# Optimization experiments

Measured on AMD Instinct MI355X. Metric: run time of the kernel, lower is better.

Reference implementation:

```python
import jax, jax.numpy as jnp
import numpy as np

B, FDIM, T, N, TOPK = 64, 80, 400, 5, 2
EPS = 1e-5


def conv2d(x, w, stride, pad):
    return jax.lax.conv_general_dilated(
        x, w, window_strides=stride,
        padding=[(pad, pad), (pad, pad)],
        dimension_numbers=('NCHW', 'OIHW', 'NCHW'))


def bn2d(x, g, b):
    # eval-mode BatchNorm2d with running_mean=0, running_var=1
    s = g / jnp.sqrt(1.0 + EPS)
    return x * s[None, :, None, None] + b[None, :, None, None]


def gelu(x):
    return jax.nn.gelu(x, approximate=False)  # torch nn.GELU default (erf)


def setup_inputs() -> dict:
    key = jax.random.key(0)
    ks = jax.random.split(key, 12)

    def rn(k, shape, scale=0.05):
        return jax.random.normal(k, shape, dtype=jnp.float32) * scale

    return {
        'x': rn(ks[0], (B, 1, FDIM, T, N), 1.0),
        'total': rn(ks[1], (B, 1, FDIM, 5 * T), 1.0),
        'gw1': rn(ks[2], (32, 1, 5, 15)),
        'g1': jnp.ones((32,), jnp.float32), 'b1': jnp.zeros((32,), jnp.float32),
        'gw2': rn(ks[3], (64, 32, 5, 15)),
        'g2': jnp.ones((64,), jnp.float32), 'b2': jnp.zeros((64,), jnp.float32),
        'gw3': rn(ks[4], (128, 64, 5, 15)),
        'g3': jnp.ones((128,), jnp.float32), 'b3': jnp.zeros((128,), jnp.float32),
        'gw4': rn(ks[5], (256, 128, 5, 15)),
        'g4': jnp.ones((256,), jnp.float32), 'b4': jnp.zeros((256,), jnp.float32),
        'fw1': rn(ks[6], (32, 256)), 'fb1': jnp.zeros((32,), jnp.float32),
        'g1d': jnp.ones((32,), jnp.float32), 'b1d': jnp.zeros((32,), jnp.float32),
        'fw2': rn(ks[7], (5, 32)), 'fb2': jnp.zeros((5,), jnp.float32),
        'cw1': rn(ks[8], (64, 1, 7, 14)),
    }


def reference(x, total, gw1, g1, b1, gw2, g2, b2, gw3, g3, b3, gw4, g4, b4,
              fw1, fb1, g1d, b1d, fw2, fb2, cw1):
    h = gelu(bn2d(conv2d(total, gw1, (2, 4), 2), g1, b1))
    h = gelu(bn2d(conv2d(h, gw2, (2, 4), 2), g2, b2))
    h = gelu(bn2d(conv2d(h, gw3, (2, 4), 2), g3, b3))
    h = gelu(bn2d(conv2d(h, gw4, (2, 4), 2), g4, b4))
    h = h.mean(axis=(2, 3))                      # AdaptiveAvgPool2d((1,1)) + Flatten -> [B,256]
    h = gelu(h @ fw1.T + fb1)                    # Linear(256,32) + GELU
    h = h * (g1d / jnp.sqrt(1.0 + EPS)) + b1d    # eval-mode BatchNorm1d(32)
    routing_weights = h @ fw2.T + fb2            # Linear(32,5) -> [B,5]

    # ---- top-k routing ----
    probs = jax.nn.softmax(routing_weights, axis=1)
    _, sel = jax.lax.top_k(probs, TOPK)          # [B,2]
    sel = jnp.sort(sel, axis=1)
    mask = jnp.transpose(jax.nn.one_hot(sel, N, dtype=x.dtype), (0, 2, 1))  # [B,5,2]

    # ---- one-hot einsum gather + reshape + stem conv ----
    gated = jnp.einsum('bcftn,bns->bcfts', x, mask)      # [B,1,80,T,2]
    gated = gated.reshape(-1, 1, FDIM, TOPK * gated.shape[3])  # [B,1,80,2T]
    out = conv2d(gated, cw1, (2, 2), 3)                  # [B,64,40,397]
    return out, routing_weights
```

## Files before the change

### kernel.cpp

```cpp
#include <hip/hip_runtime.h>
#include <hip/hip_bf16.h>

#define DEV __device__ __forceinline__

typedef __attribute__((ext_vector_type(8))) short short8_t;
typedef __attribute__((ext_vector_type(4))) float f32x4;

DEV float gelu_erf(float x) { return 0.5f * x * (1.0f + erff(x * 0.70710678118654752440f)); }
DEV ushort f2bf(float v) { __hip_bfloat16 h = __float2bfloat16(v); return *(ushort*)&h; }

DEV int xcd_swz(int bid, int nwg) {
    int q = nwg >> 3;
    return (bid & 7) * q + (bid >> 3);
}

__global__ __launch_bounds__(256) void prep_k(
    const float* __restrict__ gw1, const float* __restrict__ gw2,
    const float* __restrict__ gw3, const float* __restrict__ gw4,
    const float* __restrict__ cw1,
    ushort* __restrict__ wp1, ushort* __restrict__ wp2,
    ushort* __restrict__ wp3, ushort* __restrict__ w4p,
    ushort* __restrict__ wp5, ushort* __restrict__ zp)
{
    __shared__ float lds[9600];
    const int tid = threadIdx.x;
    int blk = blockIdx.x;
    if (blk < 256) {
        const float* src = gw4 + (size_t)blk * 9600;
        for (int i = tid; i < 9600; i += 256) lds[i] = src[i];
        __syncthreads();
        ushort* dst = w4p + (size_t)blk * 9600;
        for (int p = tid; p < 9600; p += 256) {
            int ic = p & 127, kc = p >> 7;
            dst[p] = f2bf(lds[ic * 75 + kc]);
        }
        return;
    }
    blk -= 256;
    if (blk < 128) {
        const float* src = gw3 + (size_t)blk * 4800;
        for (int i = tid; i < 4800; i += 256) lds[i] = src[i];
        __syncthreads();
        for (int p = tid; p < 4800; p += 256) {
            int ic = p & 63, kc = p >> 6;
            wp3[(size_t)kc * 8192 + blk * 64 + ic] = f2bf(lds[ic * 75 + kc]);
        }
        return;
    }
    blk -= 128;
    if (blk < 64) {
        const float* src = gw2 + (size_t)blk * 2400;
        for (int i = tid; i < 2400; i += 256) lds[i] = src[i];
        __syncthreads();
        for (int p = tid; p < 2400; p += 256) {
            int ic = p & 31, kc = p >> 5;
            wp2[(size_t)kc * 2048 + blk * 32 + ic] = f2bf(lds[ic * 75 + kc]);
        }
        return;
    }
    for (int idx = tid; idx < 3072; idx += 256) {
        int oc = idx / 96, k = idx % 96;
        int kh = k >> 4, kw = k & 15;
        float v = (kh < 5 && kw < 15) ? gw1[oc * 75 + kh * 15 + kw] : 0.f;
        wp1[idx] = f2bf(v);
    }
    for (int idx = tid; idx < 8192; idx += 256) {
        int oc = idx >> 7, k = idx & 127;
        int kh = k >> 4, t = k & 15;
        int a = t >> 1, c = t & 1, kw = 2 * a + c - 1;
        float v = (kh < 7 && kw >= 0 && kw < 14) ? cw1[oc * 98 + kh * 14 + kw] : 0.f;
        wp5[idx] = f2bf(v);
    }
    for (int idx = tid; idx < 256; idx += 256) zp[idx] = 0;
}

template <int M_BLK, int NOC, int NCH, int NWM, int NWN, int ST, bool F32IN, bool BNG>
__global__ __launch_bounds__(64 * NWM * NWN) void convmm1_k(
    const void* __restrict__ in_, const ushort* __restrict__ wp,
    const float* __restrict__ gamma, const float* __restrict__ beta,
    void* __restrict__ out_,
    int IH, int IWE, int OH, int OW, int NOWT, int PH)
{
    constexpr int NT = 64 * NWM * NWN;
    constexpr int NR = 2 * NCH;
    constexpr int SPAN = (M_BLK - 1) * ST + 16;
    constexpr int SSTR = ((SPAN + 16 + 7) & ~7) + 8;
    constexpr int STAGE_B = NR * SSTR * 2;
    constexpr int TILE_B = BNG ? (M_BLK * NOC * 2) : (NOC * M_BLK * 4);
    constexpr int SMEM_B = STAGE_B > TILE_B ? STAGE_B : TILE_B;
    constexpr int HOFF = F32IN ? 1 : 2;
    __shared__ __align__(16) char smem[SMEM_B];
    ushort* stg = (ushort*)smem;

    int bid = xcd_swz(blockIdx.x, gridDim.x);
    const int owt = bid % NOWT; bid /= NOWT;
    const int oh = bid % OH;
    const int b  = bid / OH;
    const int ow0 = owt * M_BLK;
    const int tid = threadIdx.x;
    const int w = tid >> 6, l = tid & 63;
    const int wn = w % NWN, wm = w / NWN;
    const int m_wave = wm * 32, n_wave = wn * 32;
    const int lc = l & 15, lr = l >> 4;

    if (F32IN) {
        constexpr int NG = (SPAN + 6) / 4 + 1;
        const int iwb_al = (ow0 * ST - 2) & ~3;
        const float* inf = (const float*)in_;
        for (int u = tid; u < NR * NG; u += NT) {
            int r = u / NG, gi = u - r * NG;
            int ih = oh * 2 - PH + r;
            int iw4 = iwb_al + gi * 4;
            int q = gi * 4;
            bool rowok = (unsigned)ih < (unsigned)IH;
            if (rowok && iw4 >= 0 && iw4 + 3 < IWE) {
                float4 v = *(const float4*)&inf[((size_t)b * IH + ih) * IWE + iw4];
                ushort4 h;
                h.x = f2bf(v.x); h.y = f2bf(v.y); h.z = f2bf(v.z); h.w = f2bf(v.w);
                *(ushort4*)&stg[r * SSTR + q] = h;
            } else {
#pragma unroll
                for (int j = 0; j < 4; ++j) {
                    int iw = iw4 + j;
                    float v = (rowok && (unsigned)iw < (unsigned)IWE)
                        ? inf[((size_t)b * IH + ih) * IWE + iw] : 0.f;
                    stg[r * SSTR + q + j] = f2bf(v);
                }
            }
        }
    } else {
        constexpr int SPANU = SPAN / 2;
        constexpr int NGU = (SPANU + 6) / 4 + 1;
        const int iub_al = (ow0 - 2) & ~3;
        const uint* inu = (const uint*)in_;
        for (int u = tid; u < NR * NGU; u += NT) {
            int r = u / NGU, gi = u - r * NGU;
            int ih = oh * 2 - PH + r;
            int iu4 = iub_al + gi * 4;
            bool rowok = (unsigned)ih < (unsigned)IH;
            if (rowok && iu4 >= 0 && iu4 + 3 < IWE) {
                uint4 v = *(const uint4*)&inu[((size_t)b * IH + ih) * IWE + iu4];
                *(uint4*)&stg[r * SSTR + gi * 8] = v;
            } else {
#pragma unroll
                for (int j = 0; j < 4; ++j) {
                    int iu = iu4 + j;
                    uint v = (rowok && (unsigned)iu < (unsigned)IWE)
                        ? inu[((size_t)b * IH + ih) * IWE + iu] : 0u;
                    *(uint*)&stg[r * SSTR + gi * 8 + j * 2] = v;
                }
            }
        }
    }

    short8_t bfr[NCH][2];
    {
        const ushort* wb = wp + (size_t)(n_wave + lc) * (NCH * 32) + lr * 8;
#pragma unroll
        for (int cc = 0; cc < NCH; ++cc)
#pragma unroll
            for (int nj = 0; nj < 2; ++nj)
                bfr[cc][nj] = *(const short8_t*)(wb + (size_t)nj * 16 * (NCH * 32) + cc * 32);
    }

    __syncthreads();

    f32x4 acc[2][2];
#pragma unroll
    for (int i = 0; i < 2; ++i)
#pragma unroll
        for (int j = 0; j < 2; ++j) acc[i][j] = (f32x4){0.f, 0.f, 0.f, 0.f};

#pragma unroll
    for (int cc = 0; cc < NCH; ++cc) {
        const int kh = 2 * cc + (lr >> 1);
        const uint* lrow = (const uint*)&stg[kh * SSTR];
        short8_t a[2];
#pragma unroll
        for (int mi = 0; mi < 2; ++mi) {
            const int m = m_wave + mi * 16 + lc;
            const int half = ((m * ST + (lr & 1) * 8) >> 1) + HOFF;
            union { uint u[4]; short8_t s; } av;
            av.u[0] = lrow[half];
            av.u[1] = lrow[half + 1];
            av.u[2] = lrow[half + 2];
            av.u[3] = lrow[half + 3];
            a[mi] = av.s;
        }
#pragma unroll
        for (int mi = 0; mi < 2; ++mi)
#pragma unroll
            for (int nj = 0; nj < 2; ++nj)
                acc[mi][nj] = __builtin_amdgcn_mfma_f32_16x16x32_bf16(a[mi], bfr[cc][nj], acc[mi][nj], 0, 0, 0);
    }

    __syncthreads();

    if (BNG) {
        ushort* tile = (ushort*)smem;
#pragma unroll
        for (int nj = 0; nj < 2; ++nj) {
            const int n = n_wave + nj * 16 + lc;
            const float s = gamma[n] * rsqrtf(1.0f + 1e-5f);
            const float bb = beta[n];
#pragma unroll
            for (int mi = 0; mi < 2; ++mi)
#pragma unroll
                for (int r = 0; r < 4; ++r) {
                    const int m = m_wave + mi * 16 + lr * 4 + r;
                    float y = gelu_erf(fmaf(acc[mi][nj][r], s, bb));
                    tile[m * NOC + n] = f2bf(y);
                }
        }
        __syncthreads();
        const int mv = min(M_BLK, OW - ow0);
        uint* dst = (uint*)((ushort*)out_ + (((size_t)b * OH + oh) * OW + ow0) * NOC);
        const uint* src = (const uint*)tile;
        for (int idx = tid; idx < mv * NOC / 2; idx += NT) dst[idx] = src[idx];
    } else {
        float* tile = (float*)smem;
#pragma unroll
        for (int nj = 0; nj < 2; ++nj) {
            const int n = n_wave + nj * 16 + lc;
#pragma unroll
            for (int mi = 0; mi < 2; ++mi)
#pragma unroll
                for (int r = 0; r < 4; ++r) {
                    const int m = m_wave + mi * 16 + lr * 4 + r;
                    tile[n * M_BLK + m] = acc[mi][nj][r];
                }
        }
        __syncthreads();
        const int mv = min(M_BLK, OW - ow0);
        float* outb = (float*)out_ + ((size_t)b * NOC * OH + oh) * OW + ow0;
        for (int idx = tid; idx < NOC * mv; idx += NT) {
            int oc = idx / mv, j = idx - oc * mv;
            outb[(size_t)oc * OH * OW + j] = tile[oc * M_BLK + j];
        }
    }
}

template <int M_BLK, int OC, int ICT, int NICC, int NWM, int NWN, int UNR>
__global__ __launch_bounds__(64 * NWM * NWN) void convmm_k(
    const ushort* __restrict__ in, const ushort* __restrict__ wp,
    const float* __restrict__ gamma, const float* __restrict__ beta,
    ushort* __restrict__ out,
    int IH, int IW, int OH, int OW, int NOWT)
{
    constexpr int KH = 5, KW = 15, SW = 4;
    constexpr int MI = M_BLK / (16 * NWM);
    constexpr int NJ = OC / (16 * NWN);
    constexpr int SPAN = (M_BLK - 1) * SW + KW;
    constexpr int ICB = ICT * 2;
    constexpr int NSL = ICT / 8;
    constexpr int KEYM = NSL - 1;
    constexpr int NT = 64 * NWM * NWN;
    constexpr int NUNITS = SPAN * NSL;
    constexpr int NLD = (NUNITS + NT - 1) / NT;

    __shared__ __align__(16) ushort Abuf[SPAN * ICT];

    int bid = xcd_swz(blockIdx.x, gridDim.x);
    const int owt = bid % NOWT; bid /= NOWT;
    const int oh  = bid % OH;
    const int b   = bid / OH;
    const int ow0 = owt * M_BLK;
    const int tid = threadIdx.x;
    const int w = tid >> 6, l = tid & 63;
    const int wn = w % NWN, wm = w / NWN;
    const int m_wave = wm * (16 * MI), n_wave = wn * (16 * NJ);
    const int lc = l & 15, lr = l >> 4;

    const int ih0 = oh * 2 - 2;
    const int iw0 = ow0 * SW - 2;
    const ushort* inb = in + (size_t)b * IH * IW * ICT;

    int up[NLD], usl[NLD], uoff[NLD];
    bool uv[NLD];
#pragma unroll
    for (int i = 0; i < NLD; ++i) {
        int u = tid + i * NT;
        uv[i] = u < NUNITS;
        int uu = uv[i] ? u : 0;
        up[i] = uu / NSL;
        usl[i] = uu - up[i] * NSL;
        uoff[i] = up[i] * ICB + ((usl[i] ^ ((up[i] >> 2) & KEYM)) << 4);
    }

    uint4 rg[NLD];
    auto prefetch = [&](int kh) {
        const int ih = ih0 + kh;
        const bool rowok = (unsigned)ih < (unsigned)IH;
        const ushort* src = inb + (size_t)ih * IW * ICT;
#pragma unroll
        for (int i = 0; i < NLD; ++i) {
            int iw = iw0 + up[i];
            uint4 v = {0u, 0u, 0u, 0u};
            if (rowok && uv[i] && (unsigned)iw < (unsigned)IW)
                v = *(const uint4*)(src + (size_t)iw * ICT + usl[i] * 8);
            rg[i] = v;
        }
    };
    auto writestage = [&]() {
#pragma unroll
        for (int i = 0; i < NLD; ++i)
            if (uv[i]) *(uint4*)((char*)Abuf + uoff[i]) = rg[i];
    };

    f32x4 acc[MI][NJ];
#pragma unroll
    for (int i = 0; i < MI; ++i)
#pragma unroll
        for (int j = 0; j < NJ; ++j) acc[i][j] = (f32x4){0.f, 0.f, 0.f, 0.f};

    prefetch(0);
    writestage();
    __syncthreads();

#pragma unroll 1
    for (int kh = 0; kh < KH; ++kh) {
        if (kh + 1 < KH) prefetch(kh + 1);
        const char* buf = (const char*)Abuf;
        const ushort* wkh = wp + (size_t)(kh * KW) * OC * ICT + (size_t)(n_wave + lc) * ICT + lr * 8;
#pragma unroll UNR
        for (int kw = 0; kw < KW; ++kw) {
#pragma unroll
            for (int icc = 0; icc < NICC; ++icc) {
                short8_t a[MI], bf[NJ];
#pragma unroll
                for (int mi = 0; mi < MI; ++mi) {
                    const int r = m_wave + mi * 16 + lc;
                    const int p = SW * r + kw;
                    const int sl = icc * 4 + lr;
                    a[mi] = *(const short8_t*)(buf + p * ICB + ((sl ^ ((p >> 2) & KEYM)) << 4));
                }
                const ushort* wb = wkh + (size_t)kw * OC * ICT + icc * 32;
#pragma unroll
                for (int nj = 0; nj < NJ; ++nj)
                    bf[nj] = *(const short8_t*)(wb + (size_t)nj * 16 * ICT);
#pragma unroll
                for (int mi = 0; mi < MI; ++mi)
#pragma unroll
                    for (int nj = 0; nj < NJ; ++nj)
                        acc[mi][nj] = __builtin_amdgcn_mfma_f32_16x16x32_bf16(a[mi], bf[nj], acc[mi][nj], 0, 0, 0);
            }
        }
        if (kh + 1 < KH) {
            __syncthreads();
            writestage();
            __syncthreads();
        }
    }

    ushort* outb = out + ((size_t)b * OH + oh) * OW * OC;
#pragma unroll
    for (int nj = 0; nj < NJ; ++nj) {
        const int n = n_wave + nj * 16 + lc;
        const float s = gamma[n] * rsqrtf(1.0f + 1e-5f);
        const float bb = beta[n];
#pragma unroll
        for (int mi = 0; mi < MI; ++mi) {
#pragma unroll
            for (int r = 0; r < 4; ++r) {
                const int m = m_wave + mi * 16 + lr * 4 + r;
                const int ow = ow0 + m;
                if (ow < OW) {
                    float y = gelu_erf(fmaf(acc[mi][nj][r], s, bb));
                    outb[(size_t)ow * OC + n] = f2bf(y);
                }
            }
        }
    }
}

__global__ __launch_bounds__(256) void gemm4_k(
    const ushort* __restrict__ h3, const ushort* __restrict__ Bw,
    const ushort* __restrict__ zp, float* __restrict__ part)
{
    __shared__ __align__(16) ushort Al[3][64 * 64];
    __shared__ __align__(16) ushort Bl[3][64 * 64];
    int bid = blockIdx.x;
    const int ks = bid & 7;
    const int nt = (bid >> 3) & 3;
    const int mt = bid >> 5;
    const int m0 = mt * 64, n0 = nt * 64;
    const int k0 = (ks * 150) / 8, k1 = ((ks + 1) * 150) / 8;
    const int tid = threadIdx.x;
    const int w = tid >> 6, l = tid & 63;
    const int wr = (w >> 1) * 32, wc = (w & 1) * 32;
    const int lc = l & 15, lr = l >> 4;

    int ihb[2], iwb[2], bb[2], sspo[2];
    const ushort* gbrow[2];
#pragma unroll
    for (int i = 0; i < 2; ++i) {
        int u = tid + i * 256;
        int row = u >> 3, sl = u & 7;
        int rg = m0 + row;
        int b_ = rg / 25, p = rg - b_ * 25;
        int oh = p / 5, ow = p - oh * 5;
        bb[i] = b_;
        ihb[i] = oh * 2 - 2;
        iwb[i] = ow * 4 - 2;
        sspo[i] = (sl ^ (row & 7)) * 8;
        gbrow[i] = Bw + (size_t)(n0 + row) * 9600 + sspo[i];
    }

    auto stage = [&](int kc, int buf) {
        const int kcp = kc >> 1;
        const int kh = kcp / 15, kw = kcp - kh * 15;
        const int ice = (kc & 1) * 64;
#pragma unroll
        for (int i = 0; i < 2; ++i) {
            const int ih = ihb[i] + kh, iw = iwb[i] + kw;
            const ushort* srcA = ((unsigned)ih < 10u && (unsigned)iw < 28u)
                ? h3 + ((((size_t)bb[i] * 10 + ih) * 28 + iw) << 7) + ice + sspo[i]
                : zp;
            __builtin_amdgcn_global_load_lds(srcA, &Al[buf][(tid + i * 256) * 8], 16, 0, 0);
            __builtin_amdgcn_global_load_lds(gbrow[i] + kc * 64, &Bl[buf][(tid + i * 256) * 8], 16, 0, 0);
        }
    };

    f32x4 acc[2][2];
#pragma unroll
    for (int i = 0; i < 2; ++i)
#pragma unroll
        for (int j = 0; j < 2; ++j) acc[i][j] = (f32x4){0.f, 0.f, 0.f, 0.f};

    auto compute = [&](int buf) {
        short8_t a[2][2], bq[2][2];
#pragma unroll
        for (int mi = 0; mi < 2; ++mi)
#pragma unroll
            for (int ks_ = 0; ks_ < 2; ++ks_) {
                const int row = wr + mi * 16 + lc;
                const int sl = (ks_ * 4 + lr) ^ (row & 7);
                a[mi][ks_] = *(const short8_t*)&Al[buf][row * 64 + sl * 8];
            }
#pragma unroll
        for (int nj = 0; nj < 2; ++nj)
#pragma unroll
            for (int ks_ = 0; ks_ < 2; ++ks_) {
                const int row = wc + nj * 16 + lc;
                const int sl = (ks_ * 4 + lr) ^ (row & 7);
                bq[nj][ks_] = *(const short8_t*)&Bl[buf][row * 64 + sl * 8];
            }
#pragma unroll
        for (int ks_ = 0; ks_ < 2; ++ks_)
#pragma unroll
            for (int mi = 0; mi < 2; ++mi)
#pragma unroll
                for (int nj = 0; nj < 2; ++nj)
                    acc[mi][nj] = __builtin_amdgcn_mfma_f32_16x16x32_bf16(a[mi][ks_], bq[nj][ks_], acc[mi][nj], 0, 0, 0);
    };

    stage(k0, 0); stage(k0 + 1, 1); stage(k0 + 2, 2);
    int buf = 0;
#pragma unroll 1
    for (int kc = k0; kc < k1 - 3; ++kc) {
        asm volatile("s_waitcnt vmcnt(8)" ::: "memory");
        __syncthreads();
        compute(buf);
        __syncthreads();
        stage(kc + 3, buf);
        buf = (buf == 2) ? 0 : buf + 1;
    }
    asm volatile("s_waitcnt vmcnt(8)" ::: "memory"); __syncthreads(); compute(buf); buf = (buf == 2) ? 0 : buf + 1;
    asm volatile("s_waitcnt vmcnt(4)" ::: "memory"); __syncthreads(); compute(buf); buf = (buf == 2) ? 0 : buf + 1;
    asm volatile("s_waitcnt vmcnt(0)" ::: "memory"); __syncthreads(); compute(buf);

    float* dst = part + (size_t)ks * 409600;
#pragma unroll
    for (int mi = 0; mi < 2; ++mi)
#pragma unroll
        for (int nj = 0; nj < 2; ++nj) {
            const int n = n0 + wc + 16 * nj + lc;
#pragma unroll
            for (int r = 0; r < 4; ++r) {
                const int m = m0 + wr + 16 * mi + 4 * lr + r;
                dst[(size_t)m * 256 + n] = acc[mi][nj][r];
            }
        }
}

__global__ void route_k(const float* __restrict__ part,
                        const float* __restrict__ g4, const float* __restrict__ b4,
                        const float* __restrict__ fw1, const float* __restrict__ fb1,
                        const float* __restrict__ g1d, const float* __restrict__ b1d,
                        const float* __restrict__ fw2, const float* __restrict__ fb2,
                        float* __restrict__ rw_out, int* __restrict__ sel_out)
{
    __shared__ float pooled[256];
    __shared__ float hmid[32];
    __shared__ float rwv[5];
    const int b = blockIdx.x, c = threadIdx.x;
    const float s4 = g4[c] * rsqrtf(1.0f + 1e-5f);
    const float bb4 = b4[c];
    const float* p = part + (size_t)b * 25 * 256 + c;
    float sum = 0.f;
#pragma unroll
    for (int i = 0; i < 25; ++i) {
        float v = 0.f;
#pragma unroll
        for (int j = 0; j < 8; ++j) v += p[i * 256 + j * 409600];
        sum += gelu_erf(fmaf(v, s4, bb4));
    }
    pooled[c] = sum * (1.0f / 25.0f);
    __syncthreads();
    if (c < 32) {
        float a = fb1[c];
        const float* wr = fw1 + c * 256;
        for (int i = 0; i < 256; ++i) a += pooled[i] * wr[i];
        a = gelu_erf(a);
        a = a * (g1d[c] * rsqrtf(1.0f + 1e-5f)) + b1d[c];
        hmid[c] = a;
    }
    __syncthreads();
    if (c < 5) {
        float a = fb2[c];
        const float* wr = fw2 + c * 32;
#pragma unroll
        for (int i = 0; i < 32; ++i) a += hmid[i] * wr[i];
        rwv[c] = a;
        rw_out[b * 5 + c] = a;
    }
    __syncthreads();
    if (c == 0) {
        int i1 = 0;
        for (int i = 1; i < 5; ++i) if (rwv[i] > rwv[i1]) i1 = i;
        int i2 = -1;
        for (int i = 0; i < 5; ++i) {
            if (i == i1) continue;
            if (i2 < 0 || rwv[i] > rwv[i2]) i2 = i;
        }
        sel_out[b * 2]     = i1 < i2 ? i1 : i2;
        sel_out[b * 2 + 1] = i1 < i2 ? i2 : i1;
    }
}

__global__ void gather_k(const float* __restrict__ x, const int* __restrict__ sel,
                         uint4* __restrict__ gated)
{
    const int g = blockIdx.x * blockDim.x + threadIdx.x;
    const int idx0 = g * 4;
    const int b = idx0 / 32000;
    const int s0 = sel[b * 2], s1 = sel[b * 2 + 1];
    const float* xp = x + (size_t)idx0 * 5;
    float4 v0 = *(const float4*)(xp);
    float4 v1 = *(const float4*)(xp + 4);
    float4 v2 = *(const float4*)(xp + 8);
    float4 v3 = *(const float4*)(xp + 12);
    float4 v4 = *(const float4*)(xp + 16);
    float vals[5][4];
    vals[0][0] = v0.x; vals[1][0] = v0.y; vals[2][0] = v0.z; vals[3][0] = v0.w; vals[4][0] = v1.x;
    vals[0][1] = v1.y; vals[1][1] = v1.z; vals[2][1] = v1.w; vals[3][1] = v2.x; vals[4][1] = v2.y;
    vals[0][2] = v2.z; vals[1][2] = v2.w; vals[2][2] = v3.x; vals[3][2] = v3.y; vals[4][2] = v3.z;
    vals[0][3] = v3.w; vals[1][3] = v4.x; vals[2][3] = v4.y; vals[3][3] = v4.z; vals[4][3] = v4.w;
    uint out[4];
#pragma unroll
    for (int j = 0; j < 4; ++j) {
        float lo = vals[0][j];
        lo = (s0 == 1) ? vals[1][j] : lo;
        lo = (s0 == 2) ? vals[2][j] : lo;
        lo = (s0 == 3) ? vals[3][j] : lo;
        lo = (s0 == 4) ? vals[4][j] : lo;
        float hi = vals[0][j];
        hi = (s1 == 1) ? vals[1][j] : hi;
        hi = (s1 == 2) ? vals[2][j] : hi;
        hi = (s1 == 3) ? vals[3][j] : hi;
        hi = (s1 == 4) ? vals[4][j] : hi;
        out[j] = (uint)f2bf(lo) | ((uint)f2bf(hi) << 16);
    }
    gated[g] = (uint4){out[0], out[1], out[2], out[3]};
}

extern "C" void kernel_launch(void* const* d_in, const int* in_sizes, int n_in,
                              void* d_out, int out_size, void* d_ws, size_t ws_size,
                              hipStream_t stream)
{
    const float* x     = (const float*)d_in[0];
    const float* total = (const float*)d_in[1];
    const float* gw1 = (const float*)d_in[2];
    const float* g1  = (const float*)d_in[3];
    const float* b1  = (const float*)d_in[4];
    const float* gw2 = (const float*)d_in[5];
    const float* g2  = (const float*)d_in[6];
    const float* b2  = (const float*)d_in[7];
    const float* gw3 = (const float*)d_in[8];
    const float* g3  = (const float*)d_in[9];
    const float* b3  = (const float*)d_in[10];
    const float* gw4 = (const float*)d_in[11];
    const float* g4  = (const float*)d_in[12];
    const float* b4  = (const float*)d_in[13];
    const float* fw1 = (const float*)d_in[14];
    const float* fb1 = (const float*)d_in[15];
    const float* g1d = (const float*)d_in[16];
    const float* b1d = (const float*)d_in[17];
    const float* fw2 = (const float*)d_in[18];
    const float* fb2 = (const float*)d_in[19];
    const float* cw1 = (const float*)d_in[20];

    char* ws = (char*)d_ws;
    size_t off = 0;
    auto alloc = [&](size_t bytes) { void* p = ws + off; off = (off + bytes + 255) & ~(size_t)255; return p; };
    ushort* h1n = (ushort*)alloc((size_t)40796160 * 2);
    ushort* h2n = (ushort*)alloc((size_t)9994240 * 2);
    ushort* h3n = (ushort*)alloc((size_t)2293760 * 2);
    float* part  = (float*)alloc((size_t)8 * 409600 * 4);
    int*   sel   = (int*)alloc(512);
    uint*  gated = (uint*)alloc((size_t)2048000 * 4);
    ushort* wp1 = (ushort*)alloc((size_t)3072 * 2);
    ushort* wp2 = (ushort*)alloc((size_t)153600 * 2);
    ushort* wp3 = (ushort*)alloc((size_t)614400 * 2);
    ushort* w4p = (ushort*)alloc((size_t)2457600 * 2);
    ushort* wp5 = (ushort*)alloc((size_t)8192 * 2);
    ushort* zp  = (ushort*)alloc(512);

    float* outc = (float*)d_out;
    float* rw   = outc + (size_t)65044480;

    prep_k<<<449, 256, 0, stream>>>(gw1, gw2, gw3, gw4, cw1, wp1, wp2, wp3, w4p, wp5, zp);

    convmm1_k<128, 32, 3, 4, 1, 4, true, true><<<64 * 40 * 4, 256, 0, stream>>>(
        total, wp1, g1, b1, h1n, 80, 2000, 40, 498, 4, 2);

    convmm_k<128, 64, 32, 1, 2, 2, 5><<<64 * 20, 256, 0, stream>>>(
        h1n, wp2, g2, b2, h2n, 40, 498, 20, 122, 1);

    convmm_k<32, 128, 64, 2, 1, 4, 5><<<64 * 10, 256, 0, stream>>>(
        h2n, wp3, g3, b3, h3n, 20, 122, 10, 28, 1);

    gemm4_k<<<800, 256, 0, stream>>>(h3n, w4p, zp, part);

    route_k<<<64, 256, 0, stream>>>(part, g4, b4, fw1, fb1, g1d, b1d, fw2, fb2, rw, sel);

    gather_k<<<2000, 256, 0, stream>>>(x, sel, (uint4*)gated);

    convmm1_k<64, 64, 4, 2, 2, 2, false, false><<<64 * 40 * 7, 256, 0, stream>>>(
        gated, wp5, nullptr, nullptr, outc, 80, 400, 40, 397, 7, 3);
}
```

Baseline: 433.4 us.

## Rewrite conv2/conv3 as implicit GEMM with triple-buffered async LDS loads

Replaces the per-kh row-staged conv kernels for layers 2 and 3 with an implicit-GEMM body that walks the K dimension in 32-channel chunks per tap. Each chunk's activations and weights go into a 3-deep LDS ring via global_load_lds, and hand-placed vmcnt waits let loads overlap MFMA work. Weights are now laid out per output channel (oc-major, tap, ic), and conv3 packs two output rows per block. This gives up the input reuse across kw taps inside LDS and uses smaller 128-thread blocks with fewer blocks for conv3, in exchange for a pipelined load stream.

```diff
diff --git a/kernel.cpp b/kernel.cpp
--- a/kernel.cpp
+++ b/kernel.cpp
@@ -41,9 +41,10 @@
         const float* src = gw3 + (size_t)blk * 4800;
         for (int i = tid; i < 4800; i += 256) lds[i] = src[i];
         __syncthreads();
+        ushort* dst = wp3 + (size_t)blk * 4800;
         for (int p = tid; p < 4800; p += 256) {
-            int ic = p & 63, kc = p >> 6;
-            wp3[(size_t)kc * 8192 + blk * 64 + ic] = f2bf(lds[ic * 75 + kc]);
+            int ic = p & 63, tap = p >> 6;
+            dst[p] = f2bf(lds[ic * 75 + tap]);
         }
         return;
     }
@@ -52,9 +53,10 @@
         const float* src = gw2 + (size_t)blk * 2400;
         for (int i = tid; i < 2400; i += 256) lds[i] = src[i];
         __syncthreads();
+        ushort* dst = wp2 + (size_t)blk * 2400;
         for (int p = tid; p < 2400; p += 256) {
-            int ic = p & 31, kc = p >> 5;
-            wp2[(size_t)kc * 2048 + blk * 32 + ic] = f2bf(lds[ic * 75 + kc]);
+            int ic = p & 31, tap = p >> 5;
+            dst[p] = f2bf(lds[ic * 75 + tap]);
         }
         return;
     }
@@ -240,119 +242,113 @@
     }
 }
 
-template <int M_BLK, int OC, int ICT, int NICC, int NWM, int NWN, int UNR>
-__global__ __launch_bounds__(64 * NWM * NWN) void convmm_k(
+template <int M_BLK, int NOC, int ICT, int HALVES, int OHPB, int NCH, int NWM, int NWN>
+DEV void convgemm_body(
     const ushort* __restrict__ in, const ushort* __restrict__ wp,
     const float* __restrict__ gamma, const float* __restrict__ beta,
-    ushort* __restrict__ out,
-    int IH, int IW, int OH, int OW, int NOWT)
-{
-    constexpr int KH = 5, KW = 15, SW = 4;
+    const ushort* __restrict__ zp, ushort* __restrict__ out,
+    int IH, int IW, int OH, int OW, int NBLK)
+{
+    constexpr int NT = 128;
     constexpr int MI = M_BLK / (16 * NWM);
-    constexpr int NJ = OC / (16 * NWN);
-    constexpr int SPAN = (M_BLK - 1) * SW + KW;
-    constexpr int ICB = ICT * 2;
-    constexpr int NSL = ICT / 8;
-    constexpr int KEYM = NSL - 1;
-    constexpr int NT = 64 * NWM * NWN;
-    constexpr int NUNITS = SPAN * NSL;
-    constexpr int NLD = (NUNITS + NT - 1) / NT;
-
-    __shared__ __align__(16) ushort Abuf[SPAN * ICT];
+    constexpr int NJ = NOC / (16 * NWN);
+    constexpr int KTOT = 75 * ICT;
+    constexpr int AU = M_BLK * 4 / NT;
+    constexpr int BU = NOC * 4 / NT;
+    constexpr int OWS = M_BLK / OHPB;
+    static_assert(AU + BU == 6, "vmcnt counts assume 6 loads/chunk");
+
+    __shared__ __align__(16) ushort Abuf[3][M_BLK * 32];
+    __shared__ __align__(16) ushort Bbuf[3][NOC * 32];
 
     int bid = xcd_swz(blockIdx.x, gridDim.x);
-    const int owt = bid % NOWT; bid /= NOWT;
-    const int oh  = bid % OH;
-    const int b   = bid / OH;
-    const int ow0 = owt * M_BLK;
+    const int oh0 = (bid % NBLK) * OHPB;
+    const int b   = bid / NBLK;
     const int tid = threadIdx.x;
     const int w = tid >> 6, l = tid & 63;
     const int wn = w % NWN, wm = w / NWN;
-    const int m_wave = wm * (16 * MI), n_wave = wn * (16 * NJ);
+    const int m_wave = wm * 16 * MI, n_wave = wn * 16 * NJ;
     const int lc = l & 15, lr = l >> 4;
 
-    const int ih0 = oh * 2 - 2;
-    const int iw0 = ow0 * SW - 2;
-    const ushort* inb = in + (size_t)b * IH * IW * ICT;
-
-    int up[NLD], usl[NLD], uoff[NLD];
-    bool uv[NLD];
-#pragma unroll
-    for (int i = 0; i < NLD; ++i) {
+    int aih[AU], aiw[AU];
+    const ushort* aptr[AU];
+#pragma unroll
+    for (int i = 0; i < AU; ++i) {
         int u = tid + i * NT;
-        uv[i] = u < NUNITS;
-        int uu = uv[i] ? u : 0;
-        up[i] = uu / NSL;
-        usl[i] = uu - up[i] * NSL;
-        uoff[i] = up[i] * ICB + ((usl[i] ^ ((up[i] >> 2) & KEYM)) << 4);
-    }
-
-    uint4 rg[NLD];
-    auto prefetch = [&](int kh) {
-        const int ih = ih0 + kh;
-        const bool rowok = (unsigned)ih < (unsigned)IH;
-        const ushort* src = inb + (size_t)ih * IW * ICT;
-#pragma unroll
-        for (int i = 0; i < NLD; ++i) {
-            int iw = iw0 + up[i];
-            uint4 v = {0u, 0u, 0u, 0u};
-            if (rowok && uv[i] && (unsigned)iw < (unsigned)IW)
-                v = *(const uint4*)(src + (size_t)iw * ICT + usl[i] * 8);
-            rg[i] = v;
-        }
+        int row = u >> 2, slot = u & 3;
+        int part = slot ^ ((row ^ (row >> 2)) & 3);
+        int ohp = row / OWS, owr = row - ohp * OWS;
+        aih[i] = (oh0 + ohp) * 2 - 2;
+        aiw[i] = owr * 4 - 2;
+        aptr[i] = in + (size_t)b * IH * IW * ICT + part * 8;
+    }
+    const ushort* bptr[BU];
+#pragma unroll
+    for (int i = 0; i < BU; ++i) {
+        int v = tid + i * NT;
+        int row = v >> 2, slot = v & 3;
+        int part = slot ^ ((row ^ (row >> 2)) & 3);
+        bptr[i] = wp + (size_t)row * KTOT + part * 8;
+    }
+
+    auto stage = [&](int kc, int buf) {
+        const int tap = (HALVES == 2) ? (kc >> 1) : kc;
+        const int kh = tap / 15, kw = tap - kh * 15;
+        const int ico = (HALVES == 2) ? (kc & 1) * 32 : 0;
+#pragma unroll
+        for (int i = 0; i < AU; ++i) {
+            int ih = aih[i] + kh, iw = aiw[i] + kw;
+            const ushort* src = ((unsigned)ih < (unsigned)IH && (unsigned)iw < (unsigned)IW)
+                ? aptr[i] + ((size_t)ih * IW + iw) * ICT + ico : zp;
+            __builtin_amdgcn_global_load_lds(src, &Abuf[buf][(tid + i * NT) * 8], 16, 0, 0);
+        }
+#pragma unroll
+        for (int i = 0; i < BU; ++i)
+            __builtin_amdgcn_global_load_lds(bptr[i] + kc * 32, &Bbuf[buf][(tid + i * NT) * 8], 16, 0, 0);
     };
-    auto writestage = [&]() {
-#pragma unroll
-        for (int i = 0; i < NLD; ++i)
-            if (uv[i]) *(uint4*)((char*)Abuf + uoff[i]) = rg[i];
+
+    f32x4 acc[MI][NJ];
+#pragma unroll
+    for (int i = 0; i < MI; ++i)
+#pragma unroll
+        for (int j = 0; j < NJ; ++j) acc[i][j] = (f32x4){0.f, 0.f, 0.f, 0.f};
+
+    auto compute = [&](int buf) {
+        short8_t a[MI], bq[NJ];
+#pragma unroll
+        for (int mi = 0; mi < MI; ++mi) {
+            int row = m_wave + mi * 16 + lc;
+            int sl = lr ^ ((row ^ (row >> 2)) & 3);
+            a[mi] = *(const short8_t*)&Abuf[buf][row * 32 + sl * 8];
+        }
+#pragma unroll
+        for (int nj = 0; nj < NJ; ++nj) {
+            int row = n_wave + nj * 16 + lc;
+            int sl = lr ^ ((row ^ (row >> 2)) & 3);
+            bq[nj] = *(const short8_t*)&Bbuf[buf][row * 32 + sl * 8];
+        }
+#pragma unroll
+        for (int mi = 0; mi < MI; ++mi)
+#pragma unroll
+            for (int nj = 0; nj < NJ; ++nj)
+                acc[mi][nj] = __builtin_amdgcn_mfma_f32_16x16x32_bf16(a[mi], bq[nj], acc[mi][nj], 0, 0, 0);
     };
 
-    f32x4 acc[MI][NJ];
-#pragma unroll
-    for (int i = 0; i < MI; ++i)
-#pragma unroll
-        for (int j = 0; j < NJ; ++j) acc[i][j] = (f32x4){0.f, 0.f, 0.f, 0.f};
-
-    prefetch(0);
-    writestage();
-    __syncthreads();
-
+    stage(0, 0); stage(1, 1); stage(2, 2);
+    int buf = 0;
 #pragma unroll 1
-    for (int kh = 0; kh < KH; ++kh) {
-        if (kh + 1 < KH) prefetch(kh + 1);
-        const char* buf = (const char*)Abuf;
-        const ushort* wkh = wp + (size_t)(kh * KW) * OC * ICT + (size_t)(n_wave + lc) * ICT + lr * 8;
-#pragma unroll UNR
-        for (int kw = 0; kw < KW; ++kw) {
-#pragma unroll
-            for (int icc = 0; icc < NICC; ++icc) {
-                short8_t a[MI], bf[NJ];
-#pragma unroll
-                for (int mi = 0; mi < MI; ++mi) {
-                    const int r = m_wave + mi * 16 + lc;
-                    const int p = SW * r + kw;
-                    const int sl = icc * 4 + lr;
-                    a[mi] = *(const short8_t*)(buf + p * ICB + ((sl ^ ((p >> 2) & KEYM)) << 4));
-                }
-                const ushort* wb = wkh + (size_t)kw * OC * ICT + icc * 32;
-#pragma unroll
-                for (int nj = 0; nj < NJ; ++nj)
-                    bf[nj] = *(const short8_t*)(wb + (size_t)nj * 16 * ICT);
-#pragma unroll
-                for (int mi = 0; mi < MI; ++mi)
-#pragma unroll
-                    for (int nj = 0; nj < NJ; ++nj)
-                        acc[mi][nj] = __builtin_amdgcn_mfma_f32_16x16x32_bf16(a[mi], bf[nj], acc[mi][nj], 0, 0, 0);
-            }
-        }
-        if (kh + 1 < KH) {
-            __syncthreads();
-            writestage();
-            __syncthreads();
-        }
-    }
-
-    ushort* outb = out + ((size_t)b * OH + oh) * OW * OC;
+    for (int kc = 0; kc < NCH - 3; ++kc) {
+        asm volatile("s_waitcnt vmcnt(12)" ::: "memory");
+        __syncthreads();
+        compute(buf);
+        __syncthreads();
+        stage(kc + 3, buf);
+        buf = (buf == 2) ? 0 : buf + 1;
+    }
+    asm volatile("s_waitcnt vmcnt(12)" ::: "memory"); __syncthreads(); compute(buf); buf = (buf == 2) ? 0 : buf + 1;
+    asm volatile("s_waitcnt vmcnt(6)" ::: "memory");  __syncthreads(); compute(buf); buf = (buf == 2) ? 0 : buf + 1;
+    asm volatile("s_waitcnt vmcnt(0)" ::: "memory");  __syncthreads(); compute(buf);
+
 #pragma unroll
     for (int nj = 0; nj < NJ; ++nj) {
         const int n = n_wave + nj * 16 + lc;
@@ -363,14 +359,32 @@
 #pragma unroll
             for (int r = 0; r < 4; ++r) {
                 const int m = m_wave + mi * 16 + lr * 4 + r;
-                const int ow = ow0 + m;
+                const int ohp = m / OWS, ow = m - ohp * OWS;
                 if (ow < OW) {
                     float y = gelu_erf(fmaf(acc[mi][nj][r], s, bb));
-                    outb[(size_t)ow * OC + n] = f2bf(y);
+                    out[(((size_t)b * OH + oh0 + ohp) * OW + ow) * NOC + n] = f2bf(y);
                 }
             }
         }
     }
+}
+
+__global__ __launch_bounds__(128) void convgemm2_k(
+    const ushort* __restrict__ in, const ushort* __restrict__ wp,
+    const float* __restrict__ gamma, const float* __restrict__ beta,
+    const ushort* __restrict__ zp, ushort* __restrict__ out,
+    int IH, int IW, int OH, int OW, int NBLK)
+{
+    convgemm_body<128, 64, 32, 1, 1, 75, 2, 1>(in, wp, gamma, beta, zp, out, IH, IW, OH, OW, NBLK);
+}
+
+__global__ __launch_bounds__(128) void convgemm3_k(
+    const ushort* __restrict__ in, const ushort* __restrict__ wp,
+    const float* __restrict__ gamma, const float* __restrict__ beta,
+    const ushort* __restrict__ zp, ushort* __restrict__ out,
+    int IH, int IW, int OH, int OW, int NBLK)
+{
+    convgemm_body<64, 128, 64, 2, 2, 150, 1, 2>(in, wp, gamma, beta, zp, out, IH, IW, OH, OW, NBLK);
 }
 
 __global__ __launch_bounds__(256) void gemm4_k(
@@ -624,11 +638,11 @@
     convmm1_k<128, 32, 3, 4, 1, 4, true, true><<<64 * 40 * 4, 256, 0, stream>>>(
         total, wp1, g1, b1, h1n, 80, 2000, 40, 498, 4, 2);
 
-    convmm_k<128, 64, 32, 1, 2, 2, 5><<<64 * 20, 256, 0, stream>>>(
-        h1n, wp2, g2, b2, h2n, 40, 498, 20, 122, 1);
-
-    convmm_k<32, 128, 64, 2, 1, 4, 5><<<64 * 10, 256, 0, stream>>>(
-        h2n, wp3, g3, b3, h3n, 20, 122, 10, 28, 1);
+    convgemm2_k<<<64 * 20, 128, 0, stream>>>(
+        h1n, wp2, g2, b2, zp, h2n, 40, 498, 20, 122, 20);
+
+    convgemm3_k<<<64 * 5, 128, 0, stream>>>(
+        h2n, wp3, g3, b3, zp, h3n, 20, 122, 10, 28, 5);
 
     gemm4_k<<<800, 256, 0, stream>>>(h3n, w4p, zp, part);
 
```

After: 650.2 us. 50.0% more time.
